# Performance work log

Measured on AMD Instinct MI355X. Metric: run time of the kernel, lower is better.

The kernel has to match this reference:

```python
import jax, jax.numpy as jnp
import numpy as np

NEG_SLOPE = 0.01  # torch F.leaky_relu default
N_USER = 100000
N_ITEM = 100000
N_EDGE = 640000
D = 128
N_LAYERS = 3  # 1 input + num_hidden_layers(1) + 1 output layer


def setup_inputs() -> dict:
    key = jax.random.key(0)
    ks = jax.random.split(key, 10)
    scale = 1.0 / np.sqrt(D)
    return {
        "h_user": jax.random.normal(ks[0], (N_USER, D), dtype=jnp.float32),
        "h_item": jax.random.normal(ks[1], (N_ITEM, D), dtype=jnp.float32),
        # W[layer, etype] : etype 0 = user-follows->user, 1 = user-clicks->item, 2 = item-clicked_by->user
        "W": jax.random.normal(ks[2], (N_LAYERS, 3, D, D), dtype=jnp.float32) * scale,
        "b": jnp.zeros((N_LAYERS, 3, D), dtype=jnp.float32),
        "follows_src": jax.random.randint(ks[3], (N_EDGE,), 0, N_USER, dtype=jnp.int32),
        "follows_dst": jax.random.randint(ks[4], (N_EDGE,), 0, N_USER, dtype=jnp.int32),
        "clicks_src": jax.random.randint(ks[5], (N_EDGE,), 0, N_USER, dtype=jnp.int32),
        "clicks_dst": jax.random.randint(ks[6], (N_EDGE,), 0, N_ITEM, dtype=jnp.int32),
        "cb_src": jax.random.randint(ks[7], (N_EDGE,), 0, N_ITEM, dtype=jnp.int32),
        "cb_dst": jax.random.randint(ks[8], (N_EDGE,), 0, N_USER, dtype=jnp.int32),
    }


def _etype_conv(h_src, W, b, src, dst, n_dst):
    """Per-etype Linear on src nodes, copy_u gather, mean-aggregate at dst."""
    Wh = h_src @ W + b                     # [N_src, D] dense transform (once per node)
    msg = Wh[src]                          # [E, D] gather
    s = jax.ops.segment_sum(msg, dst, num_segments=n_dst)
    cnt = jax.ops.segment_sum(jnp.ones((src.shape[0],), dtype=Wh.dtype), dst, num_segments=n_dst)
    return s / jnp.maximum(cnt, 1.0)[:, None]  # mean; isolated nodes -> 0


def _rgcn_forward(h_user, h_item, W, b, follows_src, follows_dst,
                  clicks_src, clicks_dst, cb_src, cb_dst):
    hu, hi = h_user, h_item
    for l in range(N_LAYERS):
        # per-etype mean aggregation, then cross-etype 'sum' (DGL multi_update_all)
        agg_u = (_etype_conv(hu, W[l, 0], b[l, 0], follows_src, follows_dst, N_USER)
                 + _etype_conv(hi, W[l, 2], b[l, 2], cb_src, cb_dst, N_USER))
        agg_i = _etype_conv(hu, W[l, 1], b[l, 1], clicks_src, clicks_dst, N_ITEM)
        hu = jax.nn.leaky_relu(agg_u, NEG_SLOPE)
        hi = jax.nn.leaky_relu(agg_i, NEG_SLOPE)
    return jnp.stack([hu, hi])  # [2, 100000, 128]


def reference(h_user, h_item, W, b, follows_src, follows_dst,
              clicks_src, clicks_dst, cb_src, cb_dst):
    return _rgcn_forward(h_user, h_item, W, b, follows_src, follows_dst,
                         clicks_src, clicks_dst, cb_src, cb_dst)
```

## Files before the change

### kernel.cpp

```cpp
#include <hip/hip_runtime.h>

typedef unsigned short u16;
typedef _Float16 f16;
typedef __attribute__((ext_vector_type(8))) _Float16 f16x8;
typedef __attribute__((ext_vector_type(4))) float f32x4;

#define D 128

__global__ __launch_bounds__(256) void k_convert(const float* __restrict__ in,
                                                 u16* __restrict__ out, int n8) {
  int i = blockIdx.x * 256 + threadIdx.x;
  if (i >= n8) return;
  const float4* ip = (const float4*)in;
  float4 a = ip[i * 2], b = ip[i * 2 + 1];
  f16x8 v = {(f16)a.x, (f16)a.y, (f16)a.z, (f16)a.w,
             (f16)b.x, (f16)b.y, (f16)b.z, (f16)b.w};
  *(f16x8*)(out + (size_t)i * 8) = v;
}

__global__ __launch_bounds__(256) void k_convW(const float* __restrict__ W,
                                               u16* __restrict__ Wt, int total) {
  int idx = blockIdx.x * 256 + threadIdx.x;
  if (idx >= total) return;
  int mat = idx >> 14;
  int k = (idx >> 7) & 127;
  int n = idx & 127;
  f16 v = (f16)W[idx];
  ((f16*)Wt)[(size_t)mat * 16384 + n * 128 + k] = v;
}

__global__ __launch_bounds__(256) void k_count3(
    const int* __restrict__ fd, const int* __restrict__ cd,
    const int* __restrict__ cbd, int* __restrict__ cnt,
    int NU, int NI, int nf, int nc, int ncb) {
  int e = blockIdx.x * 256 + threadIdx.x;
  if (e < nf)
    atomicAdd(&cnt[fd[e]], 1);
  else if (e < nf + nc)
    atomicAdd(&cnt[NU + cd[e - nf]], 1);
  else if (e < nf + nc + ncb)
    atomicAdd(&cnt[NU + NI + cbd[e - nf - nc]], 1);
}

__global__ __launch_bounds__(256) void k_scanA(const int* __restrict__ cnt,
                                               int* __restrict__ part, int n) {
  int t = threadIdx.x;
  int idx = blockIdx.x * 1024 + t * 4;
  int4 v = {0, 0, 0, 0};
  if (idx + 3 < n)
    v = *(const int4*)(cnt + idx);
  else {
    if (idx < n) v.x = cnt[idx];
    if (idx + 1 < n) v.y = cnt[idx + 1];
    if (idx + 2 < n) v.z = cnt[idx + 2];
    if (idx + 3 < n) v.w = cnt[idx + 3];
  }
  int s = v.x + v.y + v.z + v.w;
  for (int off = 1; off < 64; off <<= 1) s += __shfl_down(s, off, 64);
  __shared__ int ws[4];
  if ((t & 63) == 0) ws[t >> 6] = s;
  __syncthreads();
  if (t == 0) part[blockIdx.x] = ws[0] + ws[1] + ws[2] + ws[3];
}

__global__ __launch_bounds__(1024) void k_scanB(int* __restrict__ part, int n_part) {
  __shared__ int sh[1024];
  int t = threadIdx.x;
  int v = (t < n_part) ? part[t] : 0;
  sh[t] = v;
  __syncthreads();
  for (int off = 1; off < 1024; off <<= 1) {
    int u = (t >= off) ? sh[t - off] : 0;
    __syncthreads();
    sh[t] += u;
    __syncthreads();
  }
  if (t < n_part) part[t] = sh[t] - v;
}

__global__ __launch_bounds__(256) void k_scanC(const int* __restrict__ cnt,
                                               const int* __restrict__ part,
                                               int* __restrict__ rs,
                                               int n, int total) {
  int t = threadIdx.x;
  int idx = blockIdx.x * 1024 + t * 4;
  int4 v = {0, 0, 0, 0};
  if (idx + 3 < n)
    v = *(const int4*)(cnt + idx);
  else {
    if (idx < n) v.x = cnt[idx];
    if (idx + 1 < n) v.y = cnt[idx + 1];
    if (idx + 2 < n) v.z = cnt[idx + 2];
    if (idx + 3 < n) v.w = cnt[idx + 3];
  }
  int s = v.x + v.y + v.z + v.w;
  int inc = s;
  int lane = t & 63, w = t >> 6;
  for (int off = 1; off < 64; off <<= 1) {
    int u = __shfl_up(inc, off, 64);
    if (lane >= off) inc += u;
  }
  __shared__ int ws[4];
  if (lane == 63) ws[w] = inc;
  __syncthreads();
  int woff = 0;
  for (int i = 0; i < w; ++i) woff += ws[i];
  int ex = part[blockIdx.x] + woff + inc - s;
  int4 r;
  r.x = ex;
  r.y = ex + v.x;
  r.z = r.y + v.y;
  r.w = r.z + v.z;
  if (idx + 3 < n)
    *(int4*)(rs + idx) = r;
  else {
    if (idx < n) rs[idx] = r.x;
    if (idx + 1 < n) rs[idx + 1] = r.y;
    if (idx + 2 < n) rs[idx + 2] = r.z;
    if (idx + 3 < n) rs[idx + 3] = r.w;
  }
  if (blockIdx.x == 0 && t == 0) rs[n] = total;
}

__global__ __launch_bounds__(256) void k_fill3(
    const int* __restrict__ fs, const int* __restrict__ fd,
    const int* __restrict__ cs, const int* __restrict__ cd,
    const int* __restrict__ cbs, const int* __restrict__ cbd,
    const int* __restrict__ rs, int* __restrict__ cnt, int* __restrict__ csr,
    int NU, int NI, int nf, int nc, int ncb) {
  int e = blockIdx.x * 256 + threadIdx.x;
  int d, s;
  if (e < nf) {
    d = fd[e];
    s = fs[e];
  } else if (e < nf + nc) {
    d = NU + cd[e - nf];
    s = cs[e - nf];
  } else if (e < nf + nc + ncb) {
    d = NU + NI + cbd[e - nf - nc];
    s = cbs[e - nf - nc] + NU;
  } else
    return;
  int p = atomicSub(&cnt[d], 1);
  csr[rs[d] + p - 1] = s;
}

__global__ __launch_bounds__(256) void k_agg3(
    const u16* __restrict__ h_all, const int* __restrict__ csr,
    const int* __restrict__ rs, u16* __restrict__ M_all, int N3) {
  int wave = (blockIdx.x * 256 + threadIdx.x) >> 6;
  int lane = threadIdx.x & 63;
  int l16 = lane & 15;
  int w = wave * 4 + (lane >> 4);
  bool valid = w < N3;
  int wc = valid ? w : 0;
  int e = rs[wc];
  int en = valid ? rs[wc + 1] : 0;
  int deg = en - e;
  f16x8 acc0 = {0, 0, 0, 0, 0, 0, 0, 0};
  f16x8 acc1 = {0, 0, 0, 0, 0, 0, 0, 0};
  const char* hb = (const char*)h_all;
  unsigned loff = (unsigned)l16 * 16u;

  while (__any(e < en)) {
    bool a0 = e < en, a1 = e + 1 < en, a2 = e + 2 < en, a3 = e + 3 < en;
    int s0 = a0 ? csr[e] : 0;
    int s1 = a1 ? csr[e + 1] : 0;
    int s2 = a2 ? csr[e + 2] : 0;
    int s3 = a3 ? csr[e + 3] : 0;
    f16x8 v0 = {0, 0, 0, 0, 0, 0, 0, 0}, v1 = {0, 0, 0, 0, 0, 0, 0, 0};
    f16x8 v2 = {0, 0, 0, 0, 0, 0, 0, 0}, v3 = {0, 0, 0, 0, 0, 0, 0, 0};
    if (a0) v0 = *(const f16x8*)(hb + ((unsigned)s0 * 256u + loff));
    if (a1) v1 = *(const f16x8*)(hb + ((unsigned)s1 * 256u + loff));
    if (a2) v2 = *(const f16x8*)(hb + ((unsigned)s2 * 256u + loff));
    if (a3) v3 = *(const f16x8*)(hb + ((unsigned)s3 * 256u + loff));
    acc0 += v0;
    acc1 += v1;
    acc0 += v2;
    acc1 += v3;
    e += 4;
  }

  if (valid) {
    float invf = deg > 0 ? 1.0f / (float)deg : 0.f;
    f16 hinv = (f16)invf;
    f16x8 t = acc0 + acc1;
    f16x8 r = t * hinv;
    *(f16x8*)((char*)M_all + ((unsigned)wc * 256u + loff)) = r;
  }
}

template <int NE, int OUTF32>
__device__ __forceinline__ void gemm_body(
    const u16* __restrict__ mA, const u16* __restrict__ mBp,
    const u16* __restrict__ wtA, const u16* __restrict__ wtB,
    const float* __restrict__ bA, const float* __restrict__ bB,
    const int* __restrict__ rsA, const int* __restrict__ rsB,
    u16* __restrict__ o16, float* __restrict__ o32, int M, int blk) {
  int tid = threadIdx.x, lane = tid & 63, w = tid >> 6;
  int lr = lane & 15;
  int lk = (lane >> 4) * 8;
  long row0 = (long)blk * 128 + w * 32;

  f32x4 acc[2][8];
#pragma unroll
  for (int rt = 0; rt < 2; rt++)
#pragma unroll
    for (int n = 0; n < 8; n++) acc[rt][n] = (f32x4){0.f, 0.f, 0.f, 0.f};

#pragma unroll
  for (int e = 0; e < NE; ++e) {
    const f16* mm = (const f16*)((e == 0) ? mA : mBp);
    const f16* Wg = (const f16*)((e == 0) ? wtA : wtB);
#pragma unroll
    for (int ks = 0; ks < 4; ++ks) {
      int k0 = ks * 32 + lk;
      f16x8 bf[8];
#pragma unroll
      for (int n = 0; n < 8; n++) bf[n] = *(const f16x8*)(Wg + (n * 16 + lr) * D + k0);
#pragma unroll
      for (int rt = 0; rt < 2; rt++) {
        long r = row0 + rt * 16 + lr;
        if (r >= M) r = M - 1;
        f16x8 af = *(const f16x8*)(mm + r * D + k0);
#pragma unroll
        for (int n = 0; n < 8; n++)
          acc[rt][n] = __builtin_amdgcn_mfma_f32_16x16x32_f16(af, bf[n], acc[rt][n], 0, 0, 0);
      }
    }
  }

  float bAr[8], bBr[8];
#pragma unroll
  for (int n = 0; n < 8; n++) {
    bAr[n] = bA[n * 16 + lr];
    bBr[n] = (NE == 2) ? bB[n * 16 + lr] : 0.f;
  }

#pragma unroll
  for (int rt = 0; rt < 2; rt++) {
    long rbase = row0 + rt * 16 + (lane >> 4) * 4;
#pragma unroll
    for (int i = 0; i < 4; i++) {
      long r = rbase + i;
      if (r < M) {
        bool mAok = rsA[r + 1] > rsA[r];
        bool mBok = (NE == 2) && (rsB[r + 1] > rsB[r]);
#pragma unroll
        for (int n = 0; n < 8; n++) {
          int col = n * 16 + lr;
          float v = acc[rt][n][i];
          if (mAok) v += bAr[n];
          if (mBok) v += bBr[n];
          v = v > 0.f ? v : 0.01f * v;
          if (OUTF32)
            o32[r * D + col] = v;
          else
            ((f16*)o16)[r * D + col] = (f16)v;
        }
      }
    }
  }
}

template <int OUTF32>
__global__ __launch_bounds__(256) void k_gemm2(
    const u16* __restrict__ M_all, const u16* __restrict__ Wl,
    const float* __restrict__ bl, const int* __restrict__ rs_all,
    u16* __restrict__ h_all, float* __restrict__ out,
    int NU, int NI, int nbI) {
  if ((int)blockIdx.x < nbI) {
    gemm_body<1, OUTF32>(M_all + (size_t)NU * D, nullptr,
                         Wl + 16384, nullptr,
                         bl + D, nullptr,
                         rs_all + NU, nullptr,
                         h_all + (size_t)NU * D, out + (size_t)NU * D, NI,
                         blockIdx.x);
  } else {
    gemm_body<2, OUTF32>(M_all, M_all + (size_t)(NU + NI) * D,
                         Wl, Wl + 2 * 16384,
                         bl, bl + 2 * D,
                         rs_all, rs_all + NU + NI,
                         h_all, out, NU, blockIdx.x - nbI);
  }
}

extern "C" void kernel_launch(void* const* d_in, const int* in_sizes, int n_in,
                              void* d_out, int out_size, void* d_ws, size_t ws_size,
                              hipStream_t stream) {
  const float* h_user = (const float*)d_in[0];
  const float* h_item = (const float*)d_in[1];
  const float* W = (const float*)d_in[2];
  const float* bb = (const float*)d_in[3];
  const int* f_src = (const int*)d_in[4];
  const int* f_dst = (const int*)d_in[5];
  const int* c_src = (const int*)d_in[6];
  const int* c_dst = (const int*)d_in[7];
  const int* cb_src = (const int*)d_in[8];
  const int* cb_dst = (const int*)d_in[9];

  const int NU = in_sizes[0] / D;
  const int NI = in_sizes[1] / D;
  const int nEf = in_sizes[4], nEc = in_sizes[6], nEcb = in_sizes[8];
  const int N3 = NU + NI + NU;
  const int nE = nEf + nEc + nEcb;

  char* p = (char*)d_ws;
  auto alloc = [&](size_t bytes) {
    char* r = p;
    p += (bytes + 255) & ~(size_t)255;
    return r;
  };
  int* cnt_all = (int*)alloc((size_t)N3 * 4);
  int* rs_all = (int*)alloc((size_t)(N3 + 1) * 4);
  int* part = (int*)alloc(1024 * 4);
  u16* Wtg = (u16*)alloc((size_t)9 * 16384 * 2);
  int* csr_all = (int*)alloc((size_t)nE * 4);
  u16* h_all = (u16*)alloc((size_t)(NU + NI) * D * 2);
  u16* M_all = (u16*)alloc((size_t)N3 * D * 2);
  (void)ws_size;

  hipMemsetAsync(cnt_all, 0, (size_t)N3 * 4, stream);

  k_convert<<<(NU * D / 8 + 255) / 256, 256, 0, stream>>>(h_user, h_all, NU * D / 8);
  k_convert<<<(NI * D / 8 + 255) / 256, 256, 0, stream>>>(h_item, h_all + (size_t)NU * D,
                                                          NI * D / 8);
  k_convW<<<(9 * 16384 + 255) / 256, 256, 0, stream>>>(W, Wtg, 9 * 16384);

  k_count3<<<(nE + 255) / 256, 256, 0, stream>>>(f_dst, c_dst, cb_dst, cnt_all,
                                                 NU, NI, nEf, nEc, nEcb);

  int n_part = (N3 + 1023) / 1024;
  k_scanA<<<n_part, 256, 0, stream>>>(cnt_all, part, N3);
  k_scanB<<<1, 1024, 0, stream>>>(part, n_part);
  k_scanC<<<n_part, 256, 0, stream>>>(cnt_all, part, rs_all, N3, nE);

  k_fill3<<<(nE + 255) / 256, 256, 0, stream>>>(f_src, f_dst, c_src, c_dst,
                                                cb_src, cb_dst, rs_all, cnt_all,
                                                csr_all, NU, NI, nEf, nEc, nEcb);

  int nbI = (NI + 127) / 128;
  int nbU = (NU + 127) / 128;
  int agg_blocks = ((N3 + 3) / 4 + 3) / 4;

  for (int l = 0; l < 3; ++l) {
    const u16* Wl = Wtg + (size_t)l * 3 * 16384;
    const float* bl = bb + (size_t)l * 3 * D;

    k_agg3<<<agg_blocks, 256, 0, stream>>>(h_all, csr_all, rs_all, M_all, N3);

    if (l < 2)
      k_gemm2<0><<<nbI + nbU, 256, 0, stream>>>(M_all, Wl, bl, rs_all, h_all,
                                                (float*)d_out, NU, NI, nbI);
    else
      k_gemm2<1><<<nbI + nbU, 256, 0, stream>>>(M_all, Wl, bl, rs_all, h_all,
                                                (float*)d_out, NU, NI, nbI);
  }
}
```

Baseline: 625.5 us.

## Record per-edge slot in count pass and pad counters to avoid atomic contention

The counting kernel now uses the value returned by atomicAdd as each edge's slot within its destination row and stores it in a u16 array. The fill kernel then writes CSR entries directly at rs[d]+pos[e], with no second atomic pass. Counters are padded to a 64-byte stride when the workspace allows, so neighbouring destinations stop sharing cache lines during atomics. The cost is a larger memset and strided scan reads; slots stored as u16 would break if any node's degree exceeded 65535.

```diff
diff --git a/kernel.cpp b/kernel.cpp
--- a/kernel.cpp
+++ b/kernel.cpp
@@ -29,33 +29,32 @@
   ((f16*)Wt)[(size_t)mat * 16384 + n * 128 + k] = v;
 }
 
-__global__ __launch_bounds__(256) void k_count3(
+__global__ __launch_bounds__(256) void k_countpos(
     const int* __restrict__ fd, const int* __restrict__ cd,
-    const int* __restrict__ cbd, int* __restrict__ cnt,
-    int NU, int NI, int nf, int nc, int ncb) {
+    const int* __restrict__ cbd, int* __restrict__ cnt, u16* __restrict__ pos,
+    int NU, int NI, int nf, int nc, int ncb, int S) {
   int e = blockIdx.x * 256 + threadIdx.x;
+  int d;
   if (e < nf)
-    atomicAdd(&cnt[fd[e]], 1);
+    d = fd[e];
   else if (e < nf + nc)
-    atomicAdd(&cnt[NU + cd[e - nf]], 1);
+    d = NU + cd[e - nf];
   else if (e < nf + nc + ncb)
-    atomicAdd(&cnt[NU + NI + cbd[e - nf - nc]], 1);
+    d = NU + NI + cbd[e - nf - nc];
+  else
+    return;
+  int p = atomicAdd(&cnt[d * S], 1);
+  pos[e] = (u16)p;
 }
 
 __global__ __launch_bounds__(256) void k_scanA(const int* __restrict__ cnt,
-                                               int* __restrict__ part, int n) {
+                                               int* __restrict__ part, int n, int S) {
   int t = threadIdx.x;
   int idx = blockIdx.x * 1024 + t * 4;
-  int4 v = {0, 0, 0, 0};
-  if (idx + 3 < n)
-    v = *(const int4*)(cnt + idx);
-  else {
-    if (idx < n) v.x = cnt[idx];
-    if (idx + 1 < n) v.y = cnt[idx + 1];
-    if (idx + 2 < n) v.z = cnt[idx + 2];
-    if (idx + 3 < n) v.w = cnt[idx + 3];
-  }
-  int s = v.x + v.y + v.z + v.w;
+  int s = 0;
+#pragma unroll
+  for (int j = 0; j < 4; ++j)
+    if (idx + j < n) s += cnt[(idx + j) * S];
   for (int off = 1; off < 64; off <<= 1) s += __shfl_down(s, off, 64);
   __shared__ int ws[4];
   if ((t & 63) == 0) ws[t >> 6] = s;
@@ -81,19 +80,15 @@
 __global__ __launch_bounds__(256) void k_scanC(const int* __restrict__ cnt,
                                                const int* __restrict__ part,
                                                int* __restrict__ rs,
-                                               int n, int total) {
+                                               int n, int total, int S) {
   int t = threadIdx.x;
   int idx = blockIdx.x * 1024 + t * 4;
-  int4 v = {0, 0, 0, 0};
-  if (idx + 3 < n)
-    v = *(const int4*)(cnt + idx);
-  else {
-    if (idx < n) v.x = cnt[idx];
-    if (idx + 1 < n) v.y = cnt[idx + 1];
-    if (idx + 2 < n) v.z = cnt[idx + 2];
-    if (idx + 3 < n) v.w = cnt[idx + 3];
-  }
-  int s = v.x + v.y + v.z + v.w;
+  int v0 = 0, v1 = 0, v2 = 0, v3 = 0;
+  if (idx < n) v0 = cnt[idx * S];
+  if (idx + 1 < n) v1 = cnt[(idx + 1) * S];
+  if (idx + 2 < n) v2 = cnt[(idx + 2) * S];
+  if (idx + 3 < n) v3 = cnt[(idx + 3) * S];
+  int s = v0 + v1 + v2 + v3;
   int inc = s;
   int lane = t & 63, w = t >> 6;
   for (int off = 1; off < 64; off <<= 1) {
@@ -108,9 +103,9 @@
   int ex = part[blockIdx.x] + woff + inc - s;
   int4 r;
   r.x = ex;
-  r.y = ex + v.x;
-  r.z = r.y + v.y;
-  r.w = r.z + v.z;
+  r.y = ex + v0;
+  r.z = r.y + v1;
+  r.w = r.z + v2;
   if (idx + 3 < n)
     *(int4*)(rs + idx) = r;
   else {
@@ -122,12 +117,12 @@
   if (blockIdx.x == 0 && t == 0) rs[n] = total;
 }
 
-__global__ __launch_bounds__(256) void k_fill3(
+__global__ __launch_bounds__(256) void k_fillpos(
     const int* __restrict__ fs, const int* __restrict__ fd,
     const int* __restrict__ cs, const int* __restrict__ cd,
     const int* __restrict__ cbs, const int* __restrict__ cbd,
-    const int* __restrict__ rs, int* __restrict__ cnt, int* __restrict__ csr,
-    int NU, int NI, int nf, int nc, int ncb) {
+    const int* __restrict__ rs, const u16* __restrict__ pos,
+    int* __restrict__ csr, int NU, int NI, int nf, int nc, int ncb) {
   int e = blockIdx.x * 256 + threadIdx.x;
   int d, s;
   if (e < nf) {
@@ -141,8 +136,7 @@
     s = cbs[e - nf - nc] + NU;
   } else
     return;
-  int p = atomicSub(&cnt[d], 1);
-  csr[rs[d] + p - 1] = s;
+  csr[rs[d] + (int)pos[e]] = s;
 }
 
 __global__ __launch_bounds__(256) void k_agg3(
@@ -305,39 +299,44 @@
   const int N3 = NU + NI + NU;
   const int nE = nEf + nEc + nEcb;
 
+  size_t fixed = (size_t)(N3 + 1) * 4 + 1024 * 4 + (size_t)9 * 16384 * 2 +
+                 (size_t)nE * 4 + (size_t)nE * 2 +
+                 (size_t)(NU + NI) * D * 2 + (size_t)N3 * D * 2 + 4096;
+  int S = (fixed + (size_t)N3 * 64 <= ws_size) ? 16 : 1;
+
   char* p = (char*)d_ws;
   auto alloc = [&](size_t bytes) {
     char* r = p;
     p += (bytes + 255) & ~(size_t)255;
     return r;
   };
-  int* cnt_all = (int*)alloc((size_t)N3 * 4);
+  int* cnt_pad = (int*)alloc((size_t)N3 * 4 * S);
   int* rs_all = (int*)alloc((size_t)(N3 + 1) * 4);
   int* part = (int*)alloc(1024 * 4);
   u16* Wtg = (u16*)alloc((size_t)9 * 16384 * 2);
   int* csr_all = (int*)alloc((size_t)nE * 4);
+  u16* pos = (u16*)alloc((size_t)nE * 2);
   u16* h_all = (u16*)alloc((size_t)(NU + NI) * D * 2);
   u16* M_all = (u16*)alloc((size_t)N3 * D * 2);
-  (void)ws_size;
-
-  hipMemsetAsync(cnt_all, 0, (size_t)N3 * 4, stream);
+
+  hipMemsetAsync(cnt_pad, 0, (size_t)N3 * 4 * S, stream);
 
   k_convert<<<(NU * D / 8 + 255) / 256, 256, 0, stream>>>(h_user, h_all, NU * D / 8);
   k_convert<<<(NI * D / 8 + 255) / 256, 256, 0, stream>>>(h_item, h_all + (size_t)NU * D,
                                                           NI * D / 8);
   k_convW<<<(9 * 16384 + 255) / 256, 256, 0, stream>>>(W, Wtg, 9 * 16384);
 
-  k_count3<<<(nE + 255) / 256, 256, 0, stream>>>(f_dst, c_dst, cb_dst, cnt_all,
-                                                 NU, NI, nEf, nEc, nEcb);
+  k_countpos<<<(nE + 255) / 256, 256, 0, stream>>>(f_dst, c_dst, cb_dst, cnt_pad, pos,
+                                                   NU, NI, nEf, nEc, nEcb, S);
 
   int n_part = (N3 + 1023) / 1024;
-  k_scanA<<<n_part, 256, 0, stream>>>(cnt_all, part, N3);
+  k_scanA<<<n_part, 256, 0, stream>>>(cnt_pad, part, N3, S);
   k_scanB<<<1, 1024, 0, stream>>>(part, n_part);
-  k_scanC<<<n_part, 256, 0, stream>>>(cnt_all, part, rs_all, N3, nE);
-
-  k_fill3<<<(nE + 255) / 256, 256, 0, stream>>>(f_src, f_dst, c_src, c_dst,
-                                                cb_src, cb_dst, rs_all, cnt_all,
-                                                csr_all, NU, NI, nEf, nEc, nEcb);
+  k_scanC<<<n_part, 256, 0, stream>>>(cnt_pad, part, rs_all, N3, nE, S);
+
+  k_fillpos<<<(nE + 255) / 256, 256, 0, stream>>>(f_src, f_dst, c_src, c_dst,
+                                                  cb_src, cb_dst, rs_all, pos,
+                                                  csr_all, NU, NI, nEf, nEc, nEcb);
 
   int nbI = (NI + 127) / 128;
   int nbU = (NU + 127) / 128;
```

Result: faster. 577.7 us (-7.6%).
